# Optimization experiments

Hardware: AMD Instinct MI355X
Metric: run time of the kernel (lower is better)

The kernel has to match this reference:

```python
import jax, jax.numpy as jnp
import numpy as np

DIM = 256
HEADS = 8
B, H, W = 16, 80, 80
C = DIM // 4          # channels per branch = 64
DH = C // HEADS       # head dim = 8


def setup_inputs() -> dict:
    key = jax.random.key(0)
    ks = jax.random.split(key, 12)
    s = 0.02
    d = {"x": jax.random.normal(ks[0], (B, DIM, H, W), jnp.float32)}
    for i, ksz in enumerate([3, 5, 7, 9]):
        d[f"w{ksz}"] = jax.random.normal(ks[1 + i], (C, 1, ksz, ksz), jnp.float32) * s
        d[f"b{ksz}"] = jnp.zeros((C,), jnp.float32)
    d["wqkv"] = jax.random.normal(ks[5], (3 * C, C), jnp.float32) * s
    d["wproj"] = jax.random.normal(ks[6], (C, C), jnp.float32) * s
    d["bproj"] = jnp.zeros((C,), jnp.float32)
    d["wf"] = jax.random.normal(ks[7], (DIM, DIM), jnp.float32) * s
    d["bf"] = jnp.zeros((DIM,), jnp.float32)
    d["scale"] = jnp.ones((4,), jnp.float32)
    return d


def _dwconv(x, w, b):
    # depthwise conv (groups = channels) + bias + residual + relu
    y = jax.lax.conv_general_dilated(
        x, w, window_strides=(1, 1), padding="SAME",
        feature_group_count=x.shape[1],
        dimension_numbers=("NCHW", "OIHW", "NCHW"))
    return jax.nn.relu(y + b[None, :, None, None] + x)


def _linear_attention(x, wqkv, wproj, bproj):
    b, c, h, w = x.shape
    n = h * w
    t = x.reshape(b, c, n).transpose(0, 2, 1)                  # [b, n, c]
    qkv = (t @ wqkv.T).reshape(b, n, 3, HEADS, DH)
    qkv = qkv.transpose(2, 0, 3, 1, 4)                         # [3, b, h, n, dh]
    q, k, v = qkv[0], qkv[1], qkv[2]
    k = jax.nn.softmax(k, axis=-1)    # softmax over head dim
    q = jax.nn.softmax(q, axis=-2)    # softmax over tokens
    ctx = jnp.einsum("bhnd,bhne->bhde", k, v)                  # [b, h, dh, dh]
    out = jnp.einsum("bhnd,bhde->bhne", q, ctx)                # [b, h, n, dh]
    # NOTE: torch does a raw reshape [b, heads, n, dh] -> [b, n, c] (no transpose);
    # we replicate that exactly for faithfulness.
    out = out.reshape(b, n, c)
    out = out @ wproj.T + bproj
    return out.transpose(0, 2, 1).reshape(b, c, h, w)


def reference(x, w3, b3, w5, b5, w7, b7, w9, b9, wqkv, wproj, bproj, wf, bf, scale):
    sp = C
    branches = [x[:, :sp], x[:, sp:2 * sp], x[:, 2 * sp:3 * sp], x[:, 3 * sp:]]
    ws = [(w3, b3), (w5, b5), (w7, b7), (w9, b9)]
    outs = []
    for i, (xb, (wk, bk)) in enumerate(zip(branches, ws)):
        y = _dwconv(xb, wk, bk)
        y = _linear_attention(y, wqkv, wproj, bproj)
        outs.append(y * scale[i])
    cat = jnp.concatenate(outs, axis=1)                        # [b, dim, h, w]
    return jnp.einsum("bchw,oc->bohw", cat, wf) + bf[None, :, None, None]
```

## Files before the change

kernel.cpp:

```cpp
#include <hip/hip_runtime.h>
#include <hip/hip_bf16.h>
#include <cstddef>
#include <cstdint>

typedef __attribute__((ext_vector_type(8))) short short8;
typedef __attribute__((ext_vector_type(4))) float f32x4;
typedef unsigned short ushortT;

static constexpr size_t OFF_Y    = 0;
static constexpr size_t OFF_QEXP = 26214400;
static constexpr size_t OFF_CTX  = 52428800;
static constexpr size_t OFF_QS   = 52461568;
static constexpr size_t OFF_WCF  = 52465664;
static constexpr size_t OFF_WQF  = 52498432;
static constexpr size_t OFF_BC   = 52504576;

__device__ inline ushortT f2bf(float f) {
    __hip_bfloat16 h = __float2bfloat16(f);
    return *reinterpret_cast<ushortT*>(&h);
}
__device__ inline float bf2f(ushortT u) {
    __hip_bfloat16 h = *reinterpret_cast<__hip_bfloat16*>(&u);
    return __bfloat162float(h);
}

__global__ void pack_wq(const float* __restrict__ wqkv, ushortT* __restrict__ wqf) {
    int idx = blockIdx.x * 256 + threadIdx.x;
    if (idx < 12288) {
        int i = idx & 7, ln = (idx >> 3) & 63, kk = idx >> 9;
        int rt = kk >> 1, ks = kk & 1;
        int row = rt * 16 + (ln & 15), col = ks * 32 + ((ln >> 4) & 3) * 8 + i;
        wqf[idx] = f2bf(wqkv[row * 64 + col]);
    }
}

__global__ void combine_w(const float* __restrict__ wf, const float* __restrict__ wproj,
                          const float* __restrict__ bproj, const float* __restrict__ bf,
                          const float* __restrict__ scale,
                          ushortT* __restrict__ wcf, float* __restrict__ bc) {
    int o  = blockIdx.x;
    int cp = threadIdx.x;
    for (int i = 0; i < 4; i++) {
        float s = 0.f;
        for (int d = 0; d < 64; d++)
            s = fmaf(wf[o * 256 + i * 64 + d], wproj[d * 64 + cp], s);
        s *= scale[i];
        int col = i * 64 + cp;
        int mt = o >> 4, ks = col >> 5, ln = (o & 15) | (((col >> 3) & 3) << 4), ii = col & 7;
        wcf[((mt * 8 + ks) * 64 + ln) * 8 + ii] = f2bf(s);
    }
    if (cp == 0) {
        float s = bf[o];
        for (int i = 0; i < 4; i++) {
            float t = 0.f;
            for (int d = 0; d < 64; d++)
                t = fmaf(wf[o * 256 + i * 64 + d], bproj[d], t);
            s = fmaf(scale[i], t, s);
        }
        bc[o] = s;
    }
}

template<int K>
__global__ __launch_bounds__(256) void dwconv_k(const float* __restrict__ x,
    const float* __restrict__ w, const float* __restrict__ bias,
    float* __restrict__ y, int br) {
    __shared__ float tile[88 * 88];
    int b = blockIdx.x >> 6;
    int c = blockIdx.x & 63;
    int ch = br * 64 + c;
    const float* xp = x + ((size_t)b * 256 + ch) * 6400;
    for (int p = threadIdx.x; p < 88 * 88; p += 256) {
        int ty = p / 88, tx = p - (p / 88) * 88;
        int sy = ty - 4, sx = tx - 4;
        tile[p] = (sy >= 0 && sy < 80 && sx >= 0 && sx < 80) ? xp[sy * 80 + sx] : 0.f;
    }
    constexpr int R = (K - 1) / 2;
    float wr[K * K];
    #pragma unroll
    for (int q = 0; q < K * K; q++) wr[q] = w[c * K * K + q];
    float bv = bias[c];
    __syncthreads();
    float* yp = y + ((size_t)b * 256 + ch) * 6400;
    for (int p = threadIdx.x; p < 6400; p += 256) {
        int py = p / 80, px = p - (p / 80) * 80;
        float acc = bv + tile[(py + 4) * 88 + (px + 4)];
        #pragma unroll
        for (int ky = 0; ky < K; ky++)
            #pragma unroll
            for (int kx = 0; kx < K; kx++)
                acc = fmaf(wr[ky * K + kx], tile[(py + 4 - R + ky) * 88 + (px + 4 - R + kx)], acc);
        yp[p] = fmaxf(acc, 0.f);
    }
}

__global__ __launch_bounds__(256) void attn_stats(const float* __restrict__ y,
    const ushortT* __restrict__ wqf, float* __restrict__ qexp,
    float* __restrict__ ctx, float* __restrict__ qs) {
    __shared__ ushortT kv_s[4][32][136];
    int b = blockIdx.y, br = blockIdx.z;
    int w = threadIdx.x >> 6, lane = threadIdx.x & 63;
    int g = lane >> 4, c = lane & 15;
    int t0 = blockIdx.x * 256 + w * 64;
    const float* yb = y + ((size_t)b * 256 + br * 64) * 6400;
    size_t qb = (size_t)(br * 16 + b) * 409600;
    float* qsg = qs + (size_t)(br * 16 + b) * 64;
    float cacc[8];
    #pragma unroll
    for (int d = 0; d < 8; d++) cacc[d] = 0.f;
    const short8* wfp = (const short8*)wqf;

    for (int p = 0; p < 2; p++) {
        short8 byh[2][2], byl[2][2];
        #pragma unroll
        for (int tt = 0; tt < 2; tt++)
            #pragma unroll
            for (int ks = 0; ks < 2; ks++) {
                int t = t0 + p * 32 + tt * 16 + c;
                int c0 = ks * 32 + g * 8;
                short8 hi, lo;
                #pragma unroll
                for (int i = 0; i < 8; i++) {
                    float v = yb[(size_t)(c0 + i) * 6400 + t];
                    ushortT hb = f2bf(v);
                    hi[i] = (short)hb;
                    lo[i] = (short)f2bf(v - bf2f(hb));
                }
                byh[tt][ks] = hi; byl[tt][ks] = lo;
            }
        short8 a0 = wfp[0 * 64 + lane];
        short8 a1 = wfp[1 * 64 + lane];
        #pragma unroll
        for (int rt = 0; rt < 12; rt++) {
            short8 na0, na1;
            if (rt < 11) {
                na0 = wfp[((rt + 1) * 2 + 0) * 64 + lane];
                na1 = wfp[((rt + 1) * 2 + 1) * 64 + lane];
            }
            f32x4 acc[2];
            acc[0] = {0.f, 0.f, 0.f, 0.f};
            acc[1] = {0.f, 0.f, 0.f, 0.f};
            #pragma unroll
            for (int tt = 0; tt < 2; tt++) {
                acc[tt] = __builtin_amdgcn_mfma_f32_16x16x32_bf16(a0, byh[tt][0], acc[tt], 0, 0, 0);
                acc[tt] = __builtin_amdgcn_mfma_f32_16x16x32_bf16(a1, byh[tt][1], acc[tt], 0, 0, 0);
                acc[tt] = __builtin_amdgcn_mfma_f32_16x16x32_bf16(a0, byl[tt][0], acc[tt], 0, 0, 0);
                acc[tt] = __builtin_amdgcn_mfma_f32_16x16x32_bf16(a1, byl[tt][1], acc[tt], 0, 0, 0);
            }
            if (rt < 4) {
                int h = rt * 2 + (g >> 1), e0 = (g & 1) * 4;
                float qsum[4] = {0.f, 0.f, 0.f, 0.f};
                #pragma unroll
                for (int tt = 0; tt < 2; tt++) {
                    int t = t0 + p * 32 + tt * 16 + c;
                    float4 qv;
                    qv.x = __expf(acc[tt][0]); qv.y = __expf(acc[tt][1]);
                    qv.z = __expf(acc[tt][2]); qv.w = __expf(acc[tt][3]);
                    *(float4*)(qexp + qb + (size_t)h * 51200 + (size_t)t * 8 + e0) = qv;
                    qsum[0] += qv.x; qsum[1] += qv.y; qsum[2] += qv.z; qsum[3] += qv.w;
                }
                #pragma unroll
                for (int j = 0; j < 4; j++) {
                    float v = qsum[j];
                    v += __shfl_xor(v, 1); v += __shfl_xor(v, 2);
                    v += __shfl_xor(v, 4); v += __shfl_xor(v, 8);
                    if (c == 0) atomicAdd(&qsg[h * 8 + e0 + j], v);
                }
            } else {
                int kvr0 = (rt - 4) * 16 + g * 4;
                #pragma unroll
                for (int tt = 0; tt < 2; tt++) {
                    int tl = tt * 16 + c;
                    uint2 pk;
                    pk.x = (uint)f2bf(acc[tt][0]) | ((uint)f2bf(acc[tt][1]) << 16);
                    pk.y = (uint)f2bf(acc[tt][2]) | ((uint)f2bf(acc[tt][3]) << 16);
                    *(uint2*)&kv_s[w][tl][kvr0] = pk;
                }
            }
            if (rt < 11) { a0 = na0; a1 = na1; }
        }
        __syncthreads();
        {
            int tp = lane & 31, hb2 = (lane >> 5) * 4;
            #pragma unroll
            for (int hh = 0; hh < 4; hh++) {
                int h = hb2 + hh;
                ushortT* kp = &kv_s[w][tp][h * 8];
                short8 kraw = *(short8*)kp;
                float kf[8];
                #pragma unroll
                for (int e = 0; e < 8; e++) kf[e] = bf2f((ushortT)kraw[e]);
                float m = kf[0];
                #pragma unroll
                for (int e = 1; e < 8; e++) m = fmaxf(m, kf[e]);
                float ss = 0.f;
                #pragma unroll
                for (int e = 0; e < 8; e++) { kf[e] = __expf(kf[e] - m); ss += kf[e]; }
                float inv = 1.f / ss;
                short8 ko;
                #pragma unroll
                for (int e = 0; e < 8; e++) ko[e] = (short)f2bf(kf[e] * inv);
                *(short8*)kp = ko;
            }
        }
        __syncthreads();
        {
            int h2 = lane >> 3, e2 = lane & 7;
            #pragma unroll 4
            for (int t = 0; t < 32; t++) {
                float kv = bf2f(kv_s[w][t][h2 * 8 + e2]);
                short8 v8 = *(short8*)&kv_s[w][t][64 + h2 * 8];
                #pragma unroll
                for (int d = 0; d < 8; d++)
                    cacc[d] = fmaf(kv, bf2f((ushortT)v8[d]), cacc[d]);
            }
        }
        __syncthreads();
    }
    float* cg = ctx + (size_t)(br * 16 + b) * 512 + lane * 8;
    #pragma unroll
    for (int d = 0; d < 8; d++) atomicAdd(&cg[d], cacc[d]);
}

__global__ __launch_bounds__(256) void final_out(const float* __restrict__ qexp,
    const float* __restrict__ ctx, const float* __restrict__ qs,
    const ushortT* __restrict__ wcf, const float* __restrict__ bc,
    float* __restrict__ out) {
    __shared__ ushortT a_hi[64][264], a_lo[64][264];
    int b = blockIdx.y, n0 = blockIdx.x * 64;
    int w = threadIdx.x >> 6, lane = threadIdx.x & 63;
    {
        int np = n0 + lane;
        int h = np / 800, gg = np - h * 800;
        int slice = w * 16 + b;
        const float* qe = qexp + ((size_t)slice * 8 + h) * 51200 + (size_t)gg * 64;
        const float* cx = ctx + (size_t)slice * 512 + h * 64;
        const float* qv = qs + (size_t)slice * 64 + h * 8;
        float inv[8];
        #pragma unroll
        for (int e = 0; e < 8; e++) inv[e] = 1.f / qv[e];
        float cxr[64];
        #pragma unroll
        for (int q = 0; q < 64; q++) cxr[q] = cx[q] * inv[q >> 3];
        #pragma unroll
        for (int s = 0; s < 8; s++) {
            const float4* q4 = (const float4*)(qe + s * 8);
            float4 qa = q4[0], qb4 = q4[1];
            float qr[8] = {qa.x, qa.y, qa.z, qa.w, qb4.x, qb4.y, qb4.z, qb4.w};
            short8 hi, lo;
            #pragma unroll
            for (int d = 0; d < 8; d++) {
                float a = 0.f;
                #pragma unroll
                for (int e = 0; e < 8; e++) a = fmaf(qr[e], cxr[e * 8 + d], a);
                ushortT hb = f2bf(a);
                hi[d] = (short)hb;
                lo[d] = (short)f2bf(a - bf2f(hb));
            }
            int c0 = w * 64 + s * 8;
            *(short8*)&a_hi[lane][c0] = hi;
            *(short8*)&a_lo[lane][c0] = lo;
        }
    }
    __syncthreads();
    int g = lane >> 4, cc = lane & 15;
    f32x4 acc[4][4];
    #pragma unroll
    for (int m = 0; m < 4; m++)
        #pragma unroll
        for (int tt = 0; tt < 4; tt++) acc[m][tt] = {0.f, 0.f, 0.f, 0.f};
    const short8* wf8 = (const short8*)wcf;
    #pragma unroll 2
    for (int ks = 0; ks < 8; ks++) {
        short8 bh[4], bl[4];
        #pragma unroll
        for (int tt = 0; tt < 4; tt++) {
            int trow = tt * 16 + cc, c0 = ks * 32 + g * 8;
            bh[tt] = *(const short8*)&a_hi[trow][c0];
            bl[tt] = *(const short8*)&a_lo[trow][c0];
        }
        #pragma unroll
        for (int m = 0; m < 4; m++) {
            short8 aw = wf8[((size_t)(w * 4 + m) * 8 + ks) * 64 + lane];
            #pragma unroll
            for (int tt = 0; tt < 4; tt++) {
                acc[m][tt] = __builtin_amdgcn_mfma_f32_16x16x32_bf16(aw, bh[tt], acc[m][tt], 0, 0, 0);
                acc[m][tt] = __builtin_amdgcn_mfma_f32_16x16x32_bf16(aw, bl[tt], acc[m][tt], 0, 0, 0);
            }
        }
    }
    float* ob = out + (size_t)b * 256 * 6400 + n0;
    #pragma unroll
    for (int m = 0; m < 4; m++) {
        int o0 = (w * 4 + m) * 16 + g * 4;
        float bcv[4] = {bc[o0], bc[o0 + 1], bc[o0 + 2], bc[o0 + 3]};
        #pragma unroll
        for (int tt = 0; tt < 4; tt++) {
            int t = tt * 16 + cc;
            #pragma unroll
            for (int j = 0; j < 4; j++)
                ob[(size_t)(o0 + j) * 6400 + t] = acc[m][tt][j] + bcv[j];
        }
    }
}

extern "C" void kernel_launch(void* const* d_in, const int* in_sizes, int n_in,
                              void* d_out, int out_size, void* d_ws, size_t ws_size,
                              hipStream_t stream) {
    const float* x     = (const float*)d_in[0];
    const float* w3    = (const float*)d_in[1];
    const float* b3    = (const float*)d_in[2];
    const float* w5    = (const float*)d_in[3];
    const float* b5    = (const float*)d_in[4];
    const float* w7    = (const float*)d_in[5];
    const float* b7    = (const float*)d_in[6];
    const float* w9    = (const float*)d_in[7];
    const float* b9    = (const float*)d_in[8];
    const float* wqkv  = (const float*)d_in[9];
    const float* wproj = (const float*)d_in[10];
    const float* bproj = (const float*)d_in[11];
    const float* wf    = (const float*)d_in[12];
    const float* bf    = (const float*)d_in[13];
    const float* scale = (const float*)d_in[14];
    float* out = (float*)d_out;
    float* ws  = (float*)d_ws;

    hipMemsetAsync(ws + OFF_CTX, 0, (32768 + 4096) * sizeof(float), stream);

    pack_wq<<<48, 256, 0, stream>>>(wqkv, (ushortT*)(ws + OFF_WQF));
    combine_w<<<256, 64, 0, stream>>>(wf, wproj, bproj, bf, scale,
                                      (ushortT*)(ws + OFF_WCF), ws + OFF_BC);

    dwconv_k<3><<<1024, 256, 0, stream>>>(x, w3, b3, ws + OFF_Y, 0);
    dwconv_k<5><<<1024, 256, 0, stream>>>(x, w5, b5, ws + OFF_Y, 1);
    dwconv_k<7><<<1024, 256, 0, stream>>>(x, w7, b7, ws + OFF_Y, 2);
    dwconv_k<9><<<1024, 256, 0, stream>>>(x, w9, b9, ws + OFF_Y, 3);

    attn_stats<<<dim3(25, 16, 4), 256, 0, stream>>>(ws + OFF_Y,
        (const ushortT*)(ws + OFF_WQF), ws + OFF_QEXP, ws + OFF_CTX, ws + OFF_QS);

    final_out<<<dim3(100, 16), 256, 0, stream>>>(ws + OFF_QEXP, ws + OFF_CTX,
        ws + OFF_QS, (const ushortT*)(ws + OFF_WCF), ws + OFF_BC, out);
}
```

Baseline: 568.6 us.

## Recompute q in final kernel from packed bf16 y; vectorize dwconv; restructure attention

Depthwise conv now loads its tile and computes four outputs per thread using float4 accesses. The attention-stats kernel no longer writes exp(q) to global memory. Instead it writes y as hi/lo bf16 token-major arrays, fuses the k-softmax into the MFMA epilogue without block barriers, and accumulates only q column sums. A new norm_ctx kernel pre-divides ctx by the q sums, and final_out (1024 threads) recomputes q from packed y via MFMA before a swizzled-LDS projection GEMM. The aim is to cut the large fp32 qexp round trip at the cost of redundant q MFMAs and an extra launch.

```diff
diff --git a/kernel.cpp b/kernel.cpp
--- a/kernel.cpp
+++ b/kernel.cpp
@@ -8,12 +8,14 @@
 typedef unsigned short ushortT;
 
 static constexpr size_t OFF_Y    = 0;
-static constexpr size_t OFF_QEXP = 26214400;
+static constexpr size_t OFF_YHI  = 26214400;
+static constexpr size_t OFF_YLO  = 39321600;
 static constexpr size_t OFF_CTX  = 52428800;
 static constexpr size_t OFF_QS   = 52461568;
-static constexpr size_t OFF_WCF  = 52465664;
-static constexpr size_t OFF_WQF  = 52498432;
-static constexpr size_t OFF_BC   = 52504576;
+static constexpr size_t OFF_CTXN = 52465664;
+static constexpr size_t OFF_WCF  = 52498432;
+static constexpr size_t OFF_WQF  = 52531200;
+static constexpr size_t OFF_BC   = 52537344;
 
 __device__ inline ushortT f2bf(float f) {
     __hip_bfloat16 h = __float2bfloat16(f);
@@ -66,14 +68,16 @@
     const float* __restrict__ w, const float* __restrict__ bias,
     float* __restrict__ y, int br) {
     __shared__ float tile[88 * 88];
-    int b = blockIdx.x >> 6;
-    int c = blockIdx.x & 63;
+    int b = blockIdx.x >> 6, c = blockIdx.x & 63;
     int ch = br * 64 + c;
     const float* xp = x + ((size_t)b * 256 + ch) * 6400;
-    for (int p = threadIdx.x; p < 88 * 88; p += 256) {
-        int ty = p / 88, tx = p - (p / 88) * 88;
-        int sy = ty - 4, sx = tx - 4;
-        tile[p] = (sy >= 0 && sy < 80 && sx >= 0 && sx < 80) ? xp[sy * 80 + sx] : 0.f;
+    for (int idx = threadIdx.x; idx < 88 * 22; idx += 256) {
+        int r = idx / 22, c4 = idx - (idx / 22) * 22;
+        int sy = r - 4;
+        float4 v = make_float4(0.f, 0.f, 0.f, 0.f);
+        if (sy >= 0 && sy < 80 && c4 >= 1 && c4 <= 20)
+            v = *(const float4*)&xp[sy * 80 + (c4 - 1) * 4];
+        *(float4*)&tile[r * 88 + c4 * 4] = v;
     }
     constexpr int R = (K - 1) / 2;
     float wr[K * K];
@@ -82,224 +86,282 @@
     float bv = bias[c];
     __syncthreads();
     float* yp = y + ((size_t)b * 256 + ch) * 6400;
-    for (int p = threadIdx.x; p < 6400; p += 256) {
-        int py = p / 80, px = p - (p / 80) * 80;
-        float acc = bv + tile[(py + 4) * 88 + (px + 4)];
-        #pragma unroll
-        for (int ky = 0; ky < K; ky++)
-            #pragma unroll
-            for (int kx = 0; kx < K; kx++)
-                acc = fmaf(wr[ky * K + kx], tile[(py + 4 - R + ky) * 88 + (px + 4 - R + kx)], acc);
-        yp[p] = fmaxf(acc, 0.f);
-    }
-}
-
-__global__ __launch_bounds__(256) void attn_stats(const float* __restrict__ y,
-    const ushortT* __restrict__ wqf, float* __restrict__ qexp,
-    float* __restrict__ ctx, float* __restrict__ qs) {
+    for (int p4 = threadIdx.x; p4 < 1600; p4 += 256) {
+        int py = p4 / 20, px = (p4 - (p4 / 20) * 20) * 4;
+        const float* tc = &tile[(py + 4) * 88 + px + 4];
+        float4 rsd = *(const float4*)tc;
+        float a0 = bv + rsd.x, a1 = bv + rsd.y, a2 = bv + rsd.z, a3 = bv + rsd.w;
+        #pragma unroll
+        for (int ky = 0; ky < K; ky++) {
+            const float* trow = tc + (ky - R) * 88 - 4;
+            float f[12];
+            *(float4*)&f[0] = *(const float4*)&trow[0];
+            *(float4*)&f[4] = *(const float4*)&trow[4];
+            *(float4*)&f[8] = *(const float4*)&trow[8];
+            #pragma unroll
+            for (int kx = 0; kx < K; kx++) {
+                float wv = wr[ky * K + kx];
+                a0 = fmaf(wv, f[4 - R + kx + 0], a0);
+                a1 = fmaf(wv, f[4 - R + kx + 1], a1);
+                a2 = fmaf(wv, f[4 - R + kx + 2], a2);
+                a3 = fmaf(wv, f[4 - R + kx + 3], a3);
+            }
+        }
+        float4 o;
+        o.x = fmaxf(a0, 0.f); o.y = fmaxf(a1, 0.f);
+        o.z = fmaxf(a2, 0.f); o.w = fmaxf(a3, 0.f);
+        *(float4*)&yp[py * 80 + px] = o;
+    }
+}
+
+__global__ __launch_bounds__(256, 4) void attn_kv(const float* __restrict__ y,
+    const ushortT* __restrict__ wqf, ushortT* __restrict__ yhi,
+    ushortT* __restrict__ ylo, float* __restrict__ ctx, float* __restrict__ qs) {
     __shared__ ushortT kv_s[4][32][136];
     int b = blockIdx.y, br = blockIdx.z;
     int w = threadIdx.x >> 6, lane = threadIdx.x & 63;
-    int g = lane >> 4, c = lane & 15;
+    int gp = lane >> 4, c15 = lane & 15;
     int t0 = blockIdx.x * 256 + w * 64;
     const float* yb = y + ((size_t)b * 256 + br * 64) * 6400;
-    size_t qb = (size_t)(br * 16 + b) * 409600;
-    float* qsg = qs + (size_t)(br * 16 + b) * 64;
+    size_t pkb = (size_t)(b * 4 + br) * 409600;
+    const short8* wfp = (const short8*)wqf;
+
+    short8 byh[4][2], byl[4][2];
+    #pragma unroll
+    for (int tt = 0; tt < 4; tt++) {
+        int t = t0 + tt * 16 + c15;
+        #pragma unroll
+        for (int ks = 0; ks < 2; ks++) {
+            int c0 = ks * 32 + gp * 8;
+            float v[8];
+            #pragma unroll
+            for (int i = 0; i < 8; i++) v[i] = yb[(size_t)(c0 + i) * 6400 + t];
+            short8 hi, lo;
+            #pragma unroll
+            for (int i = 0; i < 8; i++) {
+                ushortT hb = f2bf(v[i]);
+                hi[i] = (short)hb;
+                lo[i] = (short)f2bf(v[i] - bf2f(hb));
+            }
+            byh[tt][ks] = hi; byl[tt][ks] = lo;
+            *(short8*)&yhi[pkb + (size_t)t * 64 + c0] = hi;
+            *(short8*)&ylo[pkb + (size_t)t * 64 + c0] = lo;
+        }
+    }
+    float qsum[16];
+    #pragma unroll
+    for (int j = 0; j < 16; j++) qsum[j] = 0.f;
+    #pragma unroll
+    for (int rt = 0; rt < 4; rt++) {
+        short8 a0 = wfp[(rt * 2 + 0) * 64 + lane];
+        short8 a1 = wfp[(rt * 2 + 1) * 64 + lane];
+        #pragma unroll
+        for (int tt = 0; tt < 4; tt++) {
+            f32x4 acc = {0.f, 0.f, 0.f, 0.f};
+            acc = __builtin_amdgcn_mfma_f32_16x16x32_bf16(a0, byh[tt][0], acc, 0, 0, 0);
+            acc = __builtin_amdgcn_mfma_f32_16x16x32_bf16(a1, byh[tt][1], acc, 0, 0, 0);
+            acc = __builtin_amdgcn_mfma_f32_16x16x32_bf16(a0, byl[tt][0], acc, 0, 0, 0);
+            acc = __builtin_amdgcn_mfma_f32_16x16x32_bf16(a1, byl[tt][1], acc, 0, 0, 0);
+            #pragma unroll
+            for (int q = 0; q < 4; q++) qsum[rt * 4 + q] += __expf(acc[q]);
+        }
+    }
+    {
+        float* qsg = qs + (size_t)(br * 16 + b) * 64;
+        #pragma unroll
+        for (int j = 0; j < 16; j++) {
+            float v = qsum[j];
+            v += __shfl_xor(v, 1); v += __shfl_xor(v, 2);
+            v += __shfl_xor(v, 4); v += __shfl_xor(v, 8);
+            if (c15 == 0) {
+                int h = 2 * (j >> 2) + (gp >> 1);
+                int e = (gp & 1) * 4 + (j & 3);
+                atomicAdd(&qsg[h * 8 + e], v);
+            }
+        }
+    }
     float cacc[8];
     #pragma unroll
     for (int d = 0; d < 8; d++) cacc[d] = 0.f;
+    int h2 = lane >> 3, e2 = lane & 7;
+    #pragma unroll
+    for (int half = 0; half < 2; half++) {
+        #pragma unroll
+        for (int rt = 0; rt < 4; rt++) {
+            short8 a0 = wfp[((rt + 4) * 2 + 0) * 64 + lane];
+            short8 a1 = wfp[((rt + 4) * 2 + 1) * 64 + lane];
+            int row0 = rt * 16 + gp * 4;
+            #pragma unroll
+            for (int tt2 = 0; tt2 < 2; tt2++) {
+                int tt = half * 2 + tt2;
+                f32x4 acc = {0.f, 0.f, 0.f, 0.f};
+                acc = __builtin_amdgcn_mfma_f32_16x16x32_bf16(a0, byh[tt][0], acc, 0, 0, 0);
+                acc = __builtin_amdgcn_mfma_f32_16x16x32_bf16(a1, byh[tt][1], acc, 0, 0, 0);
+                acc = __builtin_amdgcn_mfma_f32_16x16x32_bf16(a0, byl[tt][0], acc, 0, 0, 0);
+                acc = __builtin_amdgcn_mfma_f32_16x16x32_bf16(a1, byl[tt][1], acc, 0, 0, 0);
+                float m = fmaxf(fmaxf(acc[0], acc[1]), fmaxf(acc[2], acc[3]));
+                m = fmaxf(m, __shfl_xor(m, 16));
+                float k0 = __expf(acc[0] - m), k1 = __expf(acc[1] - m);
+                float k2v = __expf(acc[2] - m), k3 = __expf(acc[3] - m);
+                float s = k0 + k1 + k2v + k3;
+                s += __shfl_xor(s, 16);
+                float inv = 1.f / s;
+                uint2 pk;
+                pk.x = (uint)f2bf(k0 * inv) | ((uint)f2bf(k1 * inv) << 16);
+                pk.y = (uint)f2bf(k2v * inv) | ((uint)f2bf(k3 * inv) << 16);
+                *(uint2*)&kv_s[w][tt2 * 16 + c15][row0] = pk;
+            }
+        }
+        #pragma unroll
+        for (int rt = 0; rt < 4; rt++) {
+            short8 a0 = wfp[((rt + 8) * 2 + 0) * 64 + lane];
+            short8 a1 = wfp[((rt + 8) * 2 + 1) * 64 + lane];
+            int row0 = rt * 16 + gp * 4;
+            #pragma unroll
+            for (int tt2 = 0; tt2 < 2; tt2++) {
+                int tt = half * 2 + tt2;
+                f32x4 acc = {0.f, 0.f, 0.f, 0.f};
+                acc = __builtin_amdgcn_mfma_f32_16x16x32_bf16(a0, byh[tt][0], acc, 0, 0, 0);
+                acc = __builtin_amdgcn_mfma_f32_16x16x32_bf16(a1, byh[tt][1], acc, 0, 0, 0);
+                acc = __builtin_amdgcn_mfma_f32_16x16x32_bf16(a0, byl[tt][0], acc, 0, 0, 0);
+                acc = __builtin_amdgcn_mfma_f32_16x16x32_bf16(a1, byl[tt][1], acc, 0, 0, 0);
+                uint2 pk;
+                pk.x = (uint)f2bf(acc[0]) | ((uint)f2bf(acc[1]) << 16);
+                pk.y = (uint)f2bf(acc[2]) | ((uint)f2bf(acc[3]) << 16);
+                *(uint2*)&kv_s[w][tt2 * 16 + c15][64 + row0] = pk;
+            }
+        }
+        asm volatile("s_waitcnt lgkmcnt(0)" ::: "memory");
+        __builtin_amdgcn_sched_barrier(0);
+        #pragma unroll 4
+        for (int t = 0; t < 32; t++) {
+            float kv = bf2f(kv_s[w][t][h2 * 8 + e2]);
+            short8 v8 = *(short8*)&kv_s[w][t][64 + h2 * 8];
+            #pragma unroll
+            for (int d = 0; d < 8; d++)
+                cacc[d] = fmaf(kv, bf2f((ushortT)v8[d]), cacc[d]);
+        }
+        asm volatile("s_waitcnt lgkmcnt(0)" ::: "memory");
+        __builtin_amdgcn_sched_barrier(0);
+    }
+    float* cg = ctx + (size_t)(br * 16 + b) * 512 + lane * 8;
+    #pragma unroll
+    for (int d = 0; d < 8; d++) atomicAdd(&cg[d], cacc[d]);
+}
+
+__global__ void norm_ctx(const float* __restrict__ ctx, const float* __restrict__ qs,
+                         float* __restrict__ ctxn) {
+    int g = blockIdx.x, p = threadIdx.x;
+    ctxn[g * 512 + p] = ctx[g * 512 + p] / qs[g * 64 + (p >> 3)];
+}
+
+__global__ __launch_bounds__(1024) void final_out(
+    const ushortT* __restrict__ yhi, const ushortT* __restrict__ ylo,
+    const ushortT* __restrict__ wqf, const ushortT* __restrict__ wcf,
+    const float* __restrict__ ctxn, const float* __restrict__ bc,
+    float* __restrict__ out) {
+    __shared__ ushortT a_hi[128 * 264];
+    __shared__ ushortT a_lo[128 * 264];
+    int b = blockIdx.y;
+    int G0 = blockIdx.x * 16;
+    int tid = threadIdx.x;
+    int w = tid >> 6, lane = tid & 63, gp = lane >> 4, c15 = lane & 15;
+    int t0 = G0 * 8;
+
+    int mt = w & 3, ntp = w >> 2;
+    int hA = mt * 2 + (gp >> 1);
+    int eb = (gp & 1) * 4;
     const short8* wfp = (const short8*)wqf;
-
-    for (int p = 0; p < 2; p++) {
-        short8 byh[2][2], byl[2][2];
-        #pragma unroll
-        for (int tt = 0; tt < 2; tt++)
-            #pragma unroll
-            for (int ks = 0; ks < 2; ks++) {
-                int t = t0 + p * 32 + tt * 16 + c;
-                int c0 = ks * 32 + g * 8;
-                short8 hi, lo;
-                #pragma unroll
-                for (int i = 0; i < 8; i++) {
-                    float v = yb[(size_t)(c0 + i) * 6400 + t];
-                    ushortT hb = f2bf(v);
-                    hi[i] = (short)hb;
-                    lo[i] = (short)f2bf(v - bf2f(hb));
-                }
-                byh[tt][ks] = hi; byl[tt][ks] = lo;
-            }
-        short8 a0 = wfp[0 * 64 + lane];
-        short8 a1 = wfp[1 * 64 + lane];
-        #pragma unroll
-        for (int rt = 0; rt < 12; rt++) {
-            short8 na0, na1;
-            if (rt < 11) {
-                na0 = wfp[((rt + 1) * 2 + 0) * 64 + lane];
-                na1 = wfp[((rt + 1) * 2 + 1) * 64 + lane];
-            }
-            f32x4 acc[2];
-            acc[0] = {0.f, 0.f, 0.f, 0.f};
-            acc[1] = {0.f, 0.f, 0.f, 0.f};
-            #pragma unroll
-            for (int tt = 0; tt < 2; tt++) {
-                acc[tt] = __builtin_amdgcn_mfma_f32_16x16x32_bf16(a0, byh[tt][0], acc[tt], 0, 0, 0);
-                acc[tt] = __builtin_amdgcn_mfma_f32_16x16x32_bf16(a1, byh[tt][1], acc[tt], 0, 0, 0);
-                acc[tt] = __builtin_amdgcn_mfma_f32_16x16x32_bf16(a0, byl[tt][0], acc[tt], 0, 0, 0);
-                acc[tt] = __builtin_amdgcn_mfma_f32_16x16x32_bf16(a1, byl[tt][1], acc[tt], 0, 0, 0);
-            }
-            if (rt < 4) {
-                int h = rt * 2 + (g >> 1), e0 = (g & 1) * 4;
-                float qsum[4] = {0.f, 0.f, 0.f, 0.f};
-                #pragma unroll
-                for (int tt = 0; tt < 2; tt++) {
-                    int t = t0 + p * 32 + tt * 16 + c;
-                    float4 qv;
-                    qv.x = __expf(acc[tt][0]); qv.y = __expf(acc[tt][1]);
-                    qv.z = __expf(acc[tt][2]); qv.w = __expf(acc[tt][3]);
-                    *(float4*)(qexp + qb + (size_t)h * 51200 + (size_t)t * 8 + e0) = qv;
-                    qsum[0] += qv.x; qsum[1] += qv.y; qsum[2] += qv.z; qsum[3] += qv.w;
-                }
-                #pragma unroll
-                for (int j = 0; j < 4; j++) {
-                    float v = qsum[j];
-                    v += __shfl_xor(v, 1); v += __shfl_xor(v, 2);
-                    v += __shfl_xor(v, 4); v += __shfl_xor(v, 8);
-                    if (c == 0) atomicAdd(&qsg[h * 8 + e0 + j], v);
-                }
-            } else {
-                int kvr0 = (rt - 4) * 16 + g * 4;
-                #pragma unroll
-                for (int tt = 0; tt < 2; tt++) {
-                    int tl = tt * 16 + c;
-                    uint2 pk;
-                    pk.x = (uint)f2bf(acc[tt][0]) | ((uint)f2bf(acc[tt][1]) << 16);
-                    pk.y = (uint)f2bf(acc[tt][2]) | ((uint)f2bf(acc[tt][3]) << 16);
-                    *(uint2*)&kv_s[w][tl][kvr0] = pk;
-                }
-            }
-            if (rt < 11) { a0 = na0; a1 = na1; }
-        }
-        __syncthreads();
-        {
-            int tp = lane & 31, hb2 = (lane >> 5) * 4;
-            #pragma unroll
-            for (int hh = 0; hh < 4; hh++) {
-                int h = hb2 + hh;
-                ushortT* kp = &kv_s[w][tp][h * 8];
-                short8 kraw = *(short8*)kp;
-                float kf[8];
-                #pragma unroll
-                for (int e = 0; e < 8; e++) kf[e] = bf2f((ushortT)kraw[e]);
-                float m = kf[0];
-                #pragma unroll
-                for (int e = 1; e < 8; e++) m = fmaxf(m, kf[e]);
-                float ss = 0.f;
-                #pragma unroll
-                for (int e = 0; e < 8; e++) { kf[e] = __expf(kf[e] - m); ss += kf[e]; }
-                float inv = 1.f / ss;
-                short8 ko;
-                #pragma unroll
-                for (int e = 0; e < 8; e++) ko[e] = (short)f2bf(kf[e] * inv);
-                *(short8*)kp = ko;
-            }
-        }
-        __syncthreads();
-        {
-            int h2 = lane >> 3, e2 = lane & 7;
-            #pragma unroll 4
-            for (int t = 0; t < 32; t++) {
-                float kv = bf2f(kv_s[w][t][h2 * 8 + e2]);
-                short8 v8 = *(short8*)&kv_s[w][t][64 + h2 * 8];
-                #pragma unroll
-                for (int d = 0; d < 8; d++)
-                    cacc[d] = fmaf(kv, bf2f((ushortT)v8[d]), cacc[d]);
-            }
-        }
-        __syncthreads();
-    }
-    float* cg = ctx + (size_t)(br * 16 + b) * 512 + lane * 8;
-    #pragma unroll
-    for (int d = 0; d < 8; d++) atomicAdd(&cg[d], cacc[d]);
-}
-
-__global__ __launch_bounds__(256) void final_out(const float* __restrict__ qexp,
-    const float* __restrict__ ctx, const float* __restrict__ qs,
-    const ushortT* __restrict__ wcf, const float* __restrict__ bc,
-    float* __restrict__ out) {
-    __shared__ ushortT a_hi[64][264], a_lo[64][264];
-    int b = blockIdx.y, n0 = blockIdx.x * 64;
-    int w = threadIdx.x >> 6, lane = threadIdx.x & 63;
-    {
-        int np = n0 + lane;
-        int h = np / 800, gg = np - h * 800;
-        int slice = w * 16 + b;
-        const float* qe = qexp + ((size_t)slice * 8 + h) * 51200 + (size_t)gg * 64;
-        const float* cx = ctx + (size_t)slice * 512 + h * 64;
-        const float* qv = qs + (size_t)slice * 64 + h * 8;
-        float inv[8];
-        #pragma unroll
-        for (int e = 0; e < 8; e++) inv[e] = 1.f / qv[e];
-        float cxr[64];
-        #pragma unroll
-        for (int q = 0; q < 64; q++) cxr[q] = cx[q] * inv[q >> 3];
-        #pragma unroll
-        for (int s = 0; s < 8; s++) {
-            const float4* q4 = (const float4*)(qe + s * 8);
-            float4 qa = q4[0], qb4 = q4[1];
-            float qr[8] = {qa.x, qa.y, qa.z, qa.w, qb4.x, qb4.y, qb4.z, qb4.w};
-            short8 hi, lo;
+    short8 a0 = wfp[(mt * 2 + 0) * 64 + lane];
+    short8 a1 = wfp[(mt * 2 + 1) * 64 + lane];
+    for (int br = 0; br < 4; br++) {
+        const ushortT* yh = yhi + ((size_t)(b * 4 + br) * 6400 + t0) * 64;
+        const ushortT* yl = ylo + ((size_t)(b * 4 + br) * 6400 + t0) * 64;
+        const float* cx = ctxn + ((size_t)(br * 16 + b) * 8 + hA) * 64 + eb * 8;
+        float cxr[32];
+        #pragma unroll
+        for (int p = 0; p < 8; p++) {
+            float4 v4 = *(const float4*)&cx[p * 4];
+            cxr[p * 4 + 0] = v4.x; cxr[p * 4 + 1] = v4.y;
+            cxr[p * 4 + 2] = v4.z; cxr[p * 4 + 3] = v4.w;
+        }
+        #pragma unroll
+        for (int ii = 0; ii < 2; ii++) {
+            int nt = ntp * 2 + ii;
+            int tl = nt * 16 + c15;
+            short8 bh0 = *(const short8*)&yh[(size_t)tl * 64 + gp * 8];
+            short8 bh1 = *(const short8*)&yh[(size_t)tl * 64 + 32 + gp * 8];
+            short8 bl0 = *(const short8*)&yl[(size_t)tl * 64 + gp * 8];
+            short8 bl1 = *(const short8*)&yl[(size_t)tl * 64 + 32 + gp * 8];
+            f32x4 acc = {0.f, 0.f, 0.f, 0.f};
+            acc = __builtin_amdgcn_mfma_f32_16x16x32_bf16(a0, bh0, acc, 0, 0, 0);
+            acc = __builtin_amdgcn_mfma_f32_16x16x32_bf16(a1, bh1, acc, 0, 0, 0);
+            acc = __builtin_amdgcn_mfma_f32_16x16x32_bf16(a0, bl0, acc, 0, 0, 0);
+            acc = __builtin_amdgcn_mfma_f32_16x16x32_bf16(a1, bl1, acc, 0, 0, 0);
+            float qe0 = __expf(acc[0]), qe1 = __expf(acc[1]);
+            float qe2 = __expf(acc[2]), qe3 = __expf(acc[3]);
+            int gl = tl >> 3, s = tl & 7;
+            int j = hA * 16 + gl;
+            short8 hi8, lo8;
             #pragma unroll
             for (int d = 0; d < 8; d++) {
-                float a = 0.f;
-                #pragma unroll
-                for (int e = 0; e < 8; e++) a = fmaf(qr[e], cxr[e * 8 + d], a);
-                ushortT hb = f2bf(a);
-                hi[d] = (short)hb;
-                lo[d] = (short)f2bf(a - bf2f(hb));
-            }
-            int c0 = w * 64 + s * 8;
-            *(short8*)&a_hi[lane][c0] = hi;
-            *(short8*)&a_lo[lane][c0] = lo;
+                float part = qe0 * cxr[d] + qe1 * cxr[8 + d]
+                           + qe2 * cxr[16 + d] + qe3 * cxr[24 + d];
+                part += __shfl_xor(part, 16);
+                ushortT hb = f2bf(part);
+                hi8[d] = (short)hb;
+                lo8[d] = (short)f2bf(part - bf2f(hb));
+            }
+            if ((gp & 1) == 0) {
+                int cs = ((br * 8 + s) ^ (j & 7)) * 8;
+                *(short8*)&a_hi[j * 264 + cs] = hi8;
+                *(short8*)&a_lo[j * 264 + cs] = lo8;
+            }
         }
     }
     __syncthreads();
-    int g = lane >> 4, cc = lane & 15;
-    f32x4 acc[4][4];
-    #pragma unroll
-    for (int m = 0; m < 4; m++)
-        #pragma unroll
-        for (int tt = 0; tt < 4; tt++) acc[m][tt] = {0.f, 0.f, 0.f, 0.f};
-    const short8* wf8 = (const short8*)wcf;
+    int mtq = w & 3, ntp2 = w >> 2;
+    const short8* wc8 = (const short8*)wcf;
+    f32x4 acc2[4][2];
+    #pragma unroll
+    for (int mi = 0; mi < 4; mi++)
+        #pragma unroll
+        for (int ni = 0; ni < 2; ni++) acc2[mi][ni] = {0.f, 0.f, 0.f, 0.f};
     #pragma unroll 2
     for (int ks = 0; ks < 8; ks++) {
-        short8 bh[4], bl[4];
-        #pragma unroll
-        for (int tt = 0; tt < 4; tt++) {
-            int trow = tt * 16 + cc, c0 = ks * 32 + g * 8;
-            bh[tt] = *(const short8*)&a_hi[trow][c0];
-            bl[tt] = *(const short8*)&a_lo[trow][c0];
-        }
-        #pragma unroll
-        for (int m = 0; m < 4; m++) {
-            short8 aw = wf8[((size_t)(w * 4 + m) * 8 + ks) * 64 + lane];
-            #pragma unroll
-            for (int tt = 0; tt < 4; tt++) {
-                acc[m][tt] = __builtin_amdgcn_mfma_f32_16x16x32_bf16(aw, bh[tt], acc[m][tt], 0, 0, 0);
-                acc[m][tt] = __builtin_amdgcn_mfma_f32_16x16x32_bf16(aw, bl[tt], acc[m][tt], 0, 0, 0);
-            }
-        }
-    }
-    float* ob = out + (size_t)b * 256 * 6400 + n0;
-    #pragma unroll
-    for (int m = 0; m < 4; m++) {
-        int o0 = (w * 4 + m) * 16 + g * 4;
-        float bcv[4] = {bc[o0], bc[o0 + 1], bc[o0 + 2], bc[o0 + 3]};
-        #pragma unroll
-        for (int tt = 0; tt < 4; tt++) {
-            int t = tt * 16 + cc;
-            #pragma unroll
-            for (int j = 0; j < 4; j++)
-                ob[(size_t)(o0 + j) * 6400 + t] = acc[m][tt][j] + bcv[j];
+        short8 aw[4];
+        #pragma unroll
+        for (int mi = 0; mi < 4; mi++)
+            aw[mi] = wc8[(size_t)((mtq * 4 + mi) * 8 + ks) * 64 + lane];
+        short8 bh[2], bl[2];
+        #pragma unroll
+        for (int ni = 0; ni < 2; ni++) {
+            int j = (ntp2 * 2 + ni) * 16 + c15;
+            int cs = ((ks * 4 + gp) ^ (j & 7)) * 8;
+            bh[ni] = *(const short8*)&a_hi[j * 264 + cs];
+            bl[ni] = *(const short8*)&a_lo[j * 264 + cs];
+        }
+        #pragma unroll
+        for (int mi = 0; mi < 4; mi++)
+            #pragma unroll
+            for (int ni = 0; ni < 2; ni++) {
+                acc2[mi][ni] = __builtin_amdgcn_mfma_f32_16x16x32_bf16(aw[mi], bh[ni], acc2[mi][ni], 0, 0, 0);
+                acc2[mi][ni] = __builtin_amdgcn_mfma_f32_16x16x32_bf16(aw[mi], bl[ni], acc2[mi][ni], 0, 0, 0);
+            }
+    }
+    #pragma unroll
+    for (int mi = 0; mi < 4; mi++) {
+        int o = (mtq * 4 + mi) * 16 + gp * 4;
+        float b0 = bc[o], b1 = bc[o + 1], b2 = bc[o + 2], b3 = bc[o + 3];
+        #pragma unroll
+        for (int ni = 0; ni < 2; ni++) {
+            int j = (ntp2 * 2 + ni) * 16 + c15;
+            int np = (j >> 4) * 800 + G0 + (j & 15);
+            float* op = out + ((size_t)b * 256 + o) * 6400 + np;
+            op[0]          = acc2[mi][ni][0] + b0;
+            op[6400]       = acc2[mi][ni][1] + b1;
+            op[2 * 6400]   = acc2[mi][ni][2] + b2;
+            op[3 * 6400]   = acc2[mi][ni][3] + b3;
         }
     }
 }
@@ -336,9 +398,14 @@
     dwconv_k<7><<<1024, 256, 0, stream>>>(x, w7, b7, ws + OFF_Y, 2);
     dwconv_k<9><<<1024, 256, 0, stream>>>(x, w9, b9, ws + OFF_Y, 3);
 
-    attn_stats<<<dim3(25, 16, 4), 256, 0, stream>>>(ws + OFF_Y,
-        (const ushortT*)(ws + OFF_WQF), ws + OFF_QEXP, ws + OFF_CTX, ws + OFF_QS);
-
-    final_out<<<dim3(100, 16), 256, 0, stream>>>(ws + OFF_QEXP, ws + OFF_CTX,
-        ws + OFF_QS, (const ushortT*)(ws + OFF_WCF), ws + OFF_BC, out);
-}
+    attn_kv<<<dim3(25, 16, 4), 256, 0, stream>>>(ws + OFF_Y,
+        (const ushortT*)(ws + OFF_WQF), (ushortT*)(ws + OFF_YHI),
+        (ushortT*)(ws + OFF_YLO), ws + OFF_CTX, ws + OFF_QS);
+
+    norm_ctx<<<64, 512, 0, stream>>>(ws + OFF_CTX, ws + OFF_QS, ws + OFF_CTXN);
+
+    final_out<<<dim3(50, 16), 1024, 0, stream>>>(
+        (const ushortT*)(ws + OFF_YHI), (const ushortT*)(ws + OFF_YLO),
+        (const ushortT*)(ws + OFF_WQF), (const ushortT*)(ws + OFF_WCF),
+        ws + OFF_CTXN, ws + OFF_BC, out);
+}
```

After: 586.1 us. 1.03x slower.
